# Optimization experiments

Measured on AMD Instinct MI355X. Metric: run time of the kernel, lower is better.

## Reference

```python
import jax, jax.numpy as jnp
import numpy as np

N_NODES = 50000
N_EDGES = 800000
D_IN = 128
D_OUT = 128


def setup_inputs() -> dict:
    key = jax.random.key(0)
    k_x, k_e, k_w, k_b = jax.random.split(key, 4)
    x = jax.random.normal(k_x, (N_NODES, D_IN), dtype=jnp.float32)
    edge_index = jax.random.randint(k_e, (2, N_EDGES), 0, N_NODES, dtype=jnp.int64)
    # nn.Linear(in_dim, out_dim): W is [out, in], b is [out]
    W = jax.random.normal(k_w, (D_OUT, D_IN), dtype=jnp.float32) * (1.0 / np.sqrt(D_IN))
    b = jax.random.normal(k_b, (D_OUT,), dtype=jnp.float32) * 0.01
    return {"x": x, "edge_index": edge_index, "W": W, "b": b}


def reference(x, edge_index, W, b):
    row, col = edge_index[0], edge_index[1]
    n = x.shape[0]
    # scatter-add of gathered source features: agg[row] += x[col]
    agg = jax.ops.segment_sum(x[col], row, num_segments=n)  # [N, d_in]
    # in-degree per destination node (bincount of row), clamped to >= 1
    deg = jax.ops.segment_sum(jnp.ones((row.shape[0],), dtype=x.dtype), row,
                              num_segments=n)
    deg = jnp.maximum(deg, 1.0)[:, None]  # [N, 1]
    agg = agg / deg
    # linear (y = agg @ W.T + b) then relu
    return jax.nn.relu(jnp.einsum('nd,od->no', agg, W) + b)
```

## Files before the change

kernel.cpp:

```cpp
#include <hip/hip_runtime.h>

#define N_NODES 50000
#define N_EDGES 800000
#define D 128

#define NCRS 196
#define CCAP 4608
#define EPB 2048
#define NEBLK ((N_EDGES + EPB - 1) / EPB)
#define NFB 3125
#define LCAP16 768
#define XN (N_NODES * D / 4)
#define WN (D * D / 4)
#define CVTBLK ((XN + WN + 255) / 256)

#define XB_OFF   0u
#define WB_OFF   12800000u
#define GCUR_OFF 12832768u
#define CRS_OFF  12833792u
#define WS_NEED_A (CRS_OFF + (unsigned)NCRS * CCAP * 4u)

#define CNT_OFF 0u
#define OFF_OFF 200704u
#define CUR_OFF 401920u
#define CSR_OFF 602112u
#define WT_OFF  3802112u
#define PART_OFF 3867648u
#define BASE_OFF 3868672u
#define WS_NEED_B (BASE_OFF + 1024u)

#define SCAN_B 256
#define SCAN_NBLK ((N_NODES + SCAN_B - 1) / SCAN_B)

using bf16x8 = __attribute__((ext_vector_type(8))) short;
using f32x4 = __attribute__((ext_vector_type(4))) float;

static __device__ __forceinline__ unsigned short bf16_rne(float f) {
  unsigned u = __float_as_uint(f);
  return (unsigned short)((u + 0x7fffu + ((u >> 16) & 1u)) >> 16);
}
static __device__ __forceinline__ unsigned pack_bf16(float a, float b) {
  return (unsigned)bf16_rne(a) | ((unsigned)bf16_rne(b) << 16);
}
static __device__ __forceinline__ float bf_lo(unsigned v) {
  return __uint_as_float(v << 16);
}
static __device__ __forceinline__ float bf_hi(unsigned v) {
  return __uint_as_float(v & 0xffff0000u);
}

static __device__ __forceinline__ unsigned wave_excl_scan_256(
    unsigned c, int t, unsigned* wsum) {
  unsigned xinc = c;
  #pragma unroll
  for (int o = 1; o < 64; o <<= 1) {
    unsigned n = __shfl_up(xinc, o, 64);
    if ((t & 63) >= o) xinc += n;
  }
  if ((t & 63) == 63) wsum[t >> 6] = xinc;
  __syncthreads();
  unsigned add = 0;
  #pragma unroll
  for (int w = 0; w < 4; ++w)
    if (w < (t >> 6)) add += wsum[w];
  return xinc - c + add;
}

__global__ __launch_bounds__(256) void zero_gcur(unsigned* __restrict__ gcur) {
  if (threadIdx.x < NCRS) gcur[threadIdx.x] = 0u;
}

__global__ __launch_bounds__(256) void phase1(
    const float4* __restrict__ x4, uint2* __restrict__ xb,
    const float4* __restrict__ w4, uint2* __restrict__ wb,
    const int* __restrict__ ei, unsigned* __restrict__ gcur,
    unsigned* __restrict__ crs) {
  const int t = threadIdx.x;

  if (blockIdx.x < NEBLK) {
    __shared__ unsigned ent[EPB];
    __shared__ unsigned srt[EPB];
    __shared__ unsigned s[256];
    __shared__ unsigned wsum[4];
    __shared__ unsigned offx[NCRS], cur[NCRS], gb[NCRS];
    const int base = blockIdx.x * EPB;
    const int n = (N_EDGES - base < EPB) ? (N_EDGES - base) : EPB;
    for (int i = t; i < n; i += 256) {
      unsigned dst = (unsigned)ei[base + i];
      unsigned src = (unsigned)ei[N_EDGES + base + i];
      ent[i] = ((dst >> 8) << 24) | (src << 8) | (dst & 255u);
    }
    s[t] = 0;
    __syncthreads();
    for (int i = t; i < n; i += 256) atomicAdd(&s[ent[i] >> 24], 1u);
    __syncthreads();
    unsigned c = s[t];
    unsigned ex = wave_excl_scan_256(c, t, wsum);
    if (t < NCRS) {
      offx[t] = ex;
      cur[t] = ex;
      if (c) gb[t] = atomicAdd(&gcur[t], c);
    }
    __syncthreads();
    for (int i = t; i < n; i += 256) {
      unsigned e = ent[i];
      unsigned pos = atomicAdd(&cur[e >> 24], 1u);
      srt[pos] = e;
    }
    __syncthreads();
    for (int i = t; i < n; i += 256) {
      unsigned e = srt[i];
      unsigned k = e >> 24;
      unsigned idx = gb[k] + ((unsigned)i - offx[k]);
      if (idx < CCAP) crs[k * CCAP + idx] = e;
    }
  } else {
    int i = (blockIdx.x - NEBLK) * 256 + t;
    if (i < XN) {
      float4 v = x4[i];
      uint2 r;
      r.x = pack_bf16(v.x, v.y);
      r.y = pack_bf16(v.z, v.w);
      xb[i] = r;
    } else if (i < XN + WN) {
      int j = i - XN;
      float4 v = w4[j];
      uint2 r;
      r.x = pack_bf16(v.x, v.y);
      r.y = pack_bf16(v.z, v.w);
      wb[j] = r;
    }
  }
}

__global__ __launch_bounds__(256) void sortbins(
    const unsigned* __restrict__ gcur, unsigned* __restrict__ crs) {
  __shared__ unsigned ent[CCAP];
  __shared__ unsigned cur[256];
  __shared__ unsigned wsum[4];
  const int t = threadIdx.x;
  const int c = blockIdx.x;
  unsigned n = gcur[c];
  n = (n > CCAP) ? CCAP : n;
  unsigned* region = crs + (unsigned)c * CCAP;

  for (unsigned i = t; i < n; i += 256) ent[i] = region[i];
  cur[t] = 0;
  __syncthreads();
  for (unsigned i = t; i < n; i += 256) atomicAdd(&cur[ent[i] & 255u], 1u);
  __syncthreads();
  unsigned cc = cur[t];
  unsigned ex = wave_excl_scan_256(cc, t, wsum);
  unsigned* offs = region + 2304;
  offs[t] = ex;
  if (t == 255) offs[256] = n;
  __syncthreads();
  cur[t] = ex;
  __syncthreads();
  unsigned short* lst = (unsigned short*)region;
  for (unsigned i = t; i < n; i += 256) {
    unsigned e = ent[i];
    unsigned pos = atomicAdd(&cur[e & 255u], 1u);
    lst[pos] = (unsigned short)((e >> 8) & 0xFFFFu);
  }
}

__global__ __launch_bounds__(256) void agg_gemm(
    const unsigned* __restrict__ xb, const unsigned short* __restrict__ wb,
    const unsigned* __restrict__ crs, const float* __restrict__ b,
    float* __restrict__ out) {
  __shared__ unsigned abuf[16 * 64];
  __shared__ unsigned short llst[LCAP16];
  __shared__ unsigned loffs[17];
  const int t = threadIdx.x;
  const int fb = blockIdx.x;
  const int coarse = fb >> 4;
  const int ln0 = (fb & 15) * 16;

  const unsigned* region = crs + (unsigned)coarse * CCAP;
  const unsigned* offs = region + 2304;
  const unsigned short* lst = (const unsigned short*)region;

  if (t < 17) loffs[t] = offs[ln0 + t];
  __syncthreads();
  const unsigned base = loffs[0];
  unsigned total = loffs[16] - base;
  if (total > LCAP16) total = LCAP16;
  for (unsigned i = t; i < total; i += 256) llst[i] = lst[base + i];
  __syncthreads();

  const int r = t >> 4;
  const int p4 = t & 15;
  const uint4* x4g = (const uint4*)xb;
  {
    unsigned beg = loffs[r] - base, end = loffs[r + 1] - base;
    float a0 = 0.f, a1 = 0.f, a2 = 0.f, a3 = 0.f;
    float a4 = 0.f, a5 = 0.f, a6 = 0.f, a7 = 0.f;
    unsigned j = beg;
    for (; j + 8 <= end; j += 8) {
      uint4 v0 = x4g[(size_t)llst[j] * 16 + p4];
      uint4 v1 = x4g[(size_t)llst[j + 1] * 16 + p4];
      uint4 v2 = x4g[(size_t)llst[j + 2] * 16 + p4];
      uint4 v3 = x4g[(size_t)llst[j + 3] * 16 + p4];
      uint4 v4 = x4g[(size_t)llst[j + 4] * 16 + p4];
      uint4 v5 = x4g[(size_t)llst[j + 5] * 16 + p4];
      uint4 v6 = x4g[(size_t)llst[j + 6] * 16 + p4];
      uint4 v7 = x4g[(size_t)llst[j + 7] * 16 + p4];
      a0 += (bf_lo(v0.x) + bf_lo(v1.x)) + (bf_lo(v2.x) + bf_lo(v3.x)) +
            ((bf_lo(v4.x) + bf_lo(v5.x)) + (bf_lo(v6.x) + bf_lo(v7.x)));
      a1 += (bf_hi(v0.x) + bf_hi(v1.x)) + (bf_hi(v2.x) + bf_hi(v3.x)) +
            ((bf_hi(v4.x) + bf_hi(v5.x)) + (bf_hi(v6.x) + bf_hi(v7.x)));
      a2 += (bf_lo(v0.y) + bf_lo(v1.y)) + (bf_lo(v2.y) + bf_lo(v3.y)) +
            ((bf_lo(v4.y) + bf_lo(v5.y)) + (bf_lo(v6.y) + bf_lo(v7.y)));
      a3 += (bf_hi(v0.y) + bf_hi(v1.y)) + (bf_hi(v2.y) + bf_hi(v3.y)) +
            ((bf_hi(v4.y) + bf_hi(v5.y)) + (bf_hi(v6.y) + bf_hi(v7.y)));
      a4 += (bf_lo(v0.z) + bf_lo(v1.z)) + (bf_lo(v2.z) + bf_lo(v3.z)) +
            ((bf_lo(v4.z) + bf_lo(v5.z)) + (bf_lo(v6.z) + bf_lo(v7.z)));
      a5 += (bf_hi(v0.z) + bf_hi(v1.z)) + (bf_hi(v2.z) + bf_hi(v3.z)) +
            ((bf_hi(v4.z) + bf_hi(v5.z)) + (bf_hi(v6.z) + bf_hi(v7.z)));
      a6 += (bf_lo(v0.w) + bf_lo(v1.w)) + (bf_lo(v2.w) + bf_lo(v3.w)) +
            ((bf_lo(v4.w) + bf_lo(v5.w)) + (bf_lo(v6.w) + bf_lo(v7.w)));
      a7 += (bf_hi(v0.w) + bf_hi(v1.w)) + (bf_hi(v2.w) + bf_hi(v3.w)) +
            ((bf_hi(v4.w) + bf_hi(v5.w)) + (bf_hi(v6.w) + bf_hi(v7.w)));
    }
    for (; j + 2 <= end; j += 2) {
      uint4 v0 = x4g[(size_t)llst[j] * 16 + p4];
      uint4 v1 = x4g[(size_t)llst[j + 1] * 16 + p4];
      a0 += bf_lo(v0.x) + bf_lo(v1.x);
      a1 += bf_hi(v0.x) + bf_hi(v1.x);
      a2 += bf_lo(v0.y) + bf_lo(v1.y);
      a3 += bf_hi(v0.y) + bf_hi(v1.y);
      a4 += bf_lo(v0.z) + bf_lo(v1.z);
      a5 += bf_hi(v0.z) + bf_hi(v1.z);
      a6 += bf_lo(v0.w) + bf_lo(v1.w);
      a7 += bf_hi(v0.w) + bf_hi(v1.w);
    }
    if (j < end) {
      uint4 v = x4g[(size_t)llst[j] * 16 + p4];
      a0 += bf_lo(v.x);
      a1 += bf_hi(v.x);
      a2 += bf_lo(v.y);
      a3 += bf_hi(v.y);
      a4 += bf_lo(v.z);
      a5 += bf_hi(v.z);
      a6 += bf_lo(v.w);
      a7 += bf_hi(v.w);
    }
    float inv = 1.0f / fmaxf((float)(end - beg), 1.0f);
    unsigned w0 = (unsigned)(4 * p4) ^ ((unsigned)(r & 7) << 2);
    *(uint4*)&abuf[r * 64 + w0] =
        make_uint4(pack_bf16(a0 * inv, a1 * inv), pack_bf16(a2 * inv, a3 * inv),
                   pack_bf16(a4 * inv, a5 * inv), pack_bf16(a6 * inv, a7 * inv));
  }
  __syncthreads();

  const int wave = t >> 6, lane = t & 63;
  const int arow = lane & 15, khi = lane >> 4;
  bf16x8 afrag[4];
  #pragma unroll
  for (int kb = 0; kb < 4; ++kb) {
    int w0 = (kb * 16 + khi * 4) ^ ((arow & 7) << 2);
    afrag[kb] = *(const bf16x8*)&abuf[arow * 64 + w0];
  }
  #pragma unroll
  for (int ct = 0; ct < 2; ++ct) {
    int o = wave * 32 + ct * 16 + arow;
    f32x4 acc = (f32x4){0.f, 0.f, 0.f, 0.f};
    #pragma unroll
    for (int kb = 0; kb < 4; ++kb) {
      bf16x8 bfrag = *(const bf16x8*)(wb + o * 128 + kb * 32 + khi * 8);
      acc = __builtin_amdgcn_mfma_f32_16x16x32_bf16(afrag[kb], bfrag, acc,
                                                    0, 0, 0);
    }
    float bias = b[o];
    #pragma unroll
    for (int rg = 0; rg < 4; ++rg) {
      int row = fb * 16 + khi * 4 + rg;
      out[(size_t)row * 128 + o] = fmaxf(acc[rg] + bias, 0.0f);
    }
  }
}

__global__ __launch_bounds__(256) void transpose_w(
    const float* __restrict__ W, float* __restrict__ Wt) {
  int i = blockIdx.x * 256 + threadIdx.x;
  if (i < D * D) {
    int o = i >> 7, d = i & 127;
    Wt[d * D + o] = W[i];
  }
}

__global__ __launch_bounds__(256) void count_kernel(
    const int* __restrict__ ei, unsigned* __restrict__ cnt) {
  int e = blockIdx.x * 256 + threadIdx.x;
  if (e < N_EDGES) atomicAdd(&cnt[ei[e]], 1u);
}

__global__ __launch_bounds__(256) void scan_p1(
    const unsigned* __restrict__ cnt, unsigned* __restrict__ partial) {
  int t = threadIdx.x;
  int g = blockIdx.x * SCAN_B + t;
  unsigned c = (g < N_NODES) ? cnt[g] : 0u;
  #pragma unroll
  for (int o = 32; o > 0; o >>= 1) c += __shfl_down(c, o, 64);
  __shared__ unsigned ws[4];
  if ((t & 63) == 0) ws[t >> 6] = c;
  __syncthreads();
  if (t == 0) partial[blockIdx.x] = ws[0] + ws[1] + ws[2] + ws[3];
}

__global__ __launch_bounds__(256) void scan_p2(
    const unsigned* __restrict__ partial, unsigned* __restrict__ base,
    unsigned* __restrict__ off) {
  __shared__ unsigned s[256];
  int t = threadIdx.x;
  unsigned v = (t < SCAN_NBLK) ? partial[t] : 0u;
  s[t] = v;
  __syncthreads();
  #pragma unroll
  for (int o = 1; o < 256; o <<= 1) {
    unsigned a = (t >= o) ? s[t - o] : 0u;
    __syncthreads();
    s[t] += a;
    __syncthreads();
  }
  if (t < SCAN_NBLK) base[t] = s[t] - v;
  if (t == 255) off[N_NODES] = s[255];
}

__global__ __launch_bounds__(256) void scan_p3(
    const unsigned* __restrict__ cnt, const unsigned* __restrict__ base,
    unsigned* __restrict__ off, unsigned* __restrict__ cur) {
  __shared__ unsigned s[256];
  int t = threadIdx.x;
  int g = blockIdx.x * SCAN_B + t;
  unsigned c = (g < N_NODES) ? cnt[g] : 0u;
  s[t] = c;
  __syncthreads();
  #pragma unroll
  for (int o = 1; o < 256; o <<= 1) {
    unsigned a = (t >= o) ? s[t - o] : 0u;
    __syncthreads();
    s[t] += a;
    __syncthreads();
  }
  if (g < N_NODES) {
    unsigned e = base[blockIdx.x] + s[t] - c;
    off[g] = e;
    cur[g] = e;
  }
}

__global__ __launch_bounds__(256) void fill_kernel(
    const int* __restrict__ ei, unsigned* __restrict__ cur,
    int* __restrict__ csr) {
  int e = blockIdx.x * 256 + threadIdx.x;
  if (e < N_EDGES) {
    int dst = ei[e];
    int src = ei[N_EDGES + e];
    unsigned pos = atomicAdd(&cur[dst], 1u);
    csr[pos] = src;
  }
}

__global__ __launch_bounds__(256) void aggregate_kernel(
    const float* __restrict__ x, const unsigned* __restrict__ off,
    const int* __restrict__ csr, float* __restrict__ agg) {
  int wave = (blockIdx.x * 256 + threadIdx.x) >> 6;
  int lane = threadIdx.x & 63;
  if (wave >= N_NODES) return;
  unsigned beg = off[wave], end = off[wave + 1];
  const float2* x2 = (const float2*)x;
  float ax = 0.f, ay = 0.f;
  unsigned i = beg;
  for (; i + 2 <= end; i += 2) {
    int s0 = csr[i], s1 = csr[i + 1];
    float2 v0 = x2[(size_t)s0 * 64 + lane];
    float2 v1 = x2[(size_t)s1 * 64 + lane];
    ax += v0.x + v1.x;
    ay += v0.y + v1.y;
  }
  if (i < end) {
    float2 v = x2[(size_t)csr[i] * 64 + lane];
    ax += v.x;
    ay += v.y;
  }
  float inv = 1.0f / fmaxf((float)(end - beg), 1.0f);
  float2 r;
  r.x = ax * inv;
  r.y = ay * inv;
  ((float2*)agg)[(size_t)wave * 64 + lane] = r;
}

__global__ __launch_bounds__(256) void gemm_relu_kernel(
    float* __restrict__ io, const float* __restrict__ deg,
    const float* __restrict__ Wt, const float* __restrict__ b) {
  __shared__ float a_lds[32 * 128];
  int tid = threadIdx.x;
  int row0 = blockIdx.x * 32;
  const float4* g4 = (const float4*)io + (size_t)row0 * 32;
  #pragma unroll
  for (int k = 0; k < 4; ++k) {
    int f = k * 256 + tid;
    int r = f >> 5;
    int grow = row0 + r;
    float4 v = make_float4(0.f, 0.f, 0.f, 0.f);
    float inv = 1.0f;
    if (grow < N_NODES) {
      v = g4[f];
      if (deg) inv = 1.0f / fmaxf(deg[grow], 1.0f);
    }
    float* dstp = &a_lds[f * 4];
    dstp[0] = v.x * inv;
    dstp[1] = v.y * inv;
    dstp[2] = v.z * inv;
    dstp[3] = v.w * inv;
  }
  __syncthreads();
  int cq = tid & 31;
  int rb = (tid >> 5) * 4;
  float acc[4][4] = {};
  const float4* Wt4 = (const float4*)Wt;
  #pragma unroll 4
  for (int d = 0; d < 128; ++d) {
    float4 w = Wt4[d * 32 + cq];
    #pragma unroll
    for (int i = 0; i < 4; ++i) {
      float a = a_lds[(rb + i) * 128 + d];
      acc[i][0] += a * w.x;
      acc[i][1] += a * w.y;
      acc[i][2] += a * w.z;
      acc[i][3] += a * w.w;
    }
  }
  float4 bb = ((const float4*)b)[cq];
  float4* out4 = (float4*)io;
  #pragma unroll
  for (int i = 0; i < 4; ++i) {
    int grow = row0 + rb + i;
    if (grow < N_NODES) {
      float4 r;
      r.x = fmaxf(acc[i][0] + bb.x, 0.0f);
      r.y = fmaxf(acc[i][1] + bb.y, 0.0f);
      r.z = fmaxf(acc[i][2] + bb.z, 0.0f);
      r.w = fmaxf(acc[i][3] + bb.w, 0.0f);
      out4[(size_t)grow * 32 + cq] = r;
    }
  }
}

__global__ __launch_bounds__(256) void scatter_kernel(
    const float* __restrict__ x, const int* __restrict__ ei,
    float* __restrict__ agg, float* __restrict__ deg) {
  int gid = blockIdx.x * 256 + threadIdx.x;
  int e = gid >> 5;
  if (e >= N_EDGES) return;
  int part = gid & 31;
  int dst = ei[e];
  int src = ei[N_EDGES + e];
  const float4* x4 = (const float4*)x;
  float4 v = x4[(size_t)src * 32 + part];
  float* base = agg + (size_t)dst * D + part * 4;
  atomicAdd(base + 0, v.x);
  atomicAdd(base + 1, v.y);
  atomicAdd(base + 2, v.z);
  atomicAdd(base + 3, v.w);
  if (part == 0) atomicAdd(deg + dst, 1.0f);
}

extern "C" void kernel_launch(void* const* d_in, const int* in_sizes, int n_in,
                              void* d_out, int out_size, void* d_ws, size_t ws_size,
                              hipStream_t stream) {
  const float* x = (const float*)d_in[0];
  const int* ei = (const int*)d_in[1];
  const float* W = (const float*)d_in[2];
  const float* b = (const float*)d_in[3];
  float* out = (float*)d_out;

  if (ws_size >= WS_NEED_A) {
    unsigned* xb = (unsigned*)((char*)d_ws + XB_OFF);
    unsigned short* wb = (unsigned short*)((char*)d_ws + WB_OFF);
    unsigned* gcur = (unsigned*)((char*)d_ws + GCUR_OFF);
    unsigned* crs = (unsigned*)((char*)d_ws + CRS_OFF);

    zero_gcur<<<1, 256, 0, stream>>>(gcur);
    phase1<<<NEBLK + CVTBLK, 256, 0, stream>>>(
        (const float4*)x, (uint2*)xb, (const float4*)W, (uint2*)wb,
        ei, gcur, crs);
    sortbins<<<NCRS, 256, 0, stream>>>(gcur, crs);
    agg_gemm<<<NFB, 256, 0, stream>>>(xb, wb, crs, b, out);
  } else if (ws_size >= WS_NEED_B) {
    unsigned* cnt = (unsigned*)((char*)d_ws + CNT_OFF);
    unsigned* off = (unsigned*)((char*)d_ws + OFF_OFF);
    unsigned* cur = (unsigned*)((char*)d_ws + CUR_OFF);
    int* csr = (int*)((char*)d_ws + CSR_OFF);
    float* Wt = (float*)((char*)d_ws + WT_OFF);
    unsigned* partial = (unsigned*)((char*)d_ws + PART_OFF);
    unsigned* base = (unsigned*)((char*)d_ws + BASE_OFF);

    hipMemsetAsync(cnt, 0, N_NODES * sizeof(unsigned), stream);
    transpose_w<<<(D * D + 255) / 256, 256, 0, stream>>>(W, Wt);
    count_kernel<<<(N_EDGES + 255) / 256, 256, 0, stream>>>(ei, cnt);
    scan_p1<<<SCAN_NBLK, 256, 0, stream>>>(cnt, partial);
    scan_p2<<<1, 256, 0, stream>>>(partial, base, off);
    scan_p3<<<SCAN_NBLK, 256, 0, stream>>>(cnt, base, off, cur);
    fill_kernel<<<(N_EDGES + 255) / 256, 256, 0, stream>>>(ei, cur, csr);
    aggregate_kernel<<<(N_NODES * 64 + 255) / 256, 256, 0, stream>>>(
        x, off, csr, out);
    gemm_relu_kernel<<<(N_NODES + 31) / 32, 256, 0, stream>>>(
        out, nullptr, Wt, b);
  } else {
    float* deg = (float*)d_ws;
    float* Wt = (float*)((char*)d_ws + 256 * 1024);
    hipMemsetAsync(d_out, 0, (size_t)N_NODES * D * sizeof(float), stream);
    hipMemsetAsync(deg, 0, N_NODES * sizeof(float), stream);
    transpose_w<<<(D * D + 255) / 256, 256, 0, stream>>>(W, Wt);
    scatter_kernel<<<(N_EDGES * 32) / 256, 256, 0, stream>>>(x, ei, out, deg);
    gemm_relu_kernel<<<(N_NODES + 31) / 32, 256, 0, stream>>>(out, deg, Wt, b);
  }
}
```

Baseline: 70.46 us.

## Split bf16 conversion across binning and sort kernels to balance load

The fp32-to-bf16 conversion of x and W, previously done entirely in the binning kernel, is now split. The first 2048 blocks' worth of items stay in the binning kernel and the rest move into extra blocks of the per-bin sort kernel. The sort kernel has only 196 blocks and would otherwise leave most of the GPU idle, so the moved work can fill those idle compute units. The cost is a heavier sort launch, and the sort blocks may now queue behind conversion blocks.

```diff
diff --git a/kernel.cpp b/kernel.cpp
--- a/kernel.cpp
+++ b/kernel.cpp
@@ -12,7 +12,11 @@
 #define LCAP16 768
 #define XN (N_NODES * D / 4)
 #define WN (D * D / 4)
-#define CVTBLK ((XN + WN + 255) / 256)
+#define CVT_TOT (XN + WN)
+#define CVTA_BLK 2048
+#define CVTA_ITEMS (CVTA_BLK * 256)
+#define CVTB_ITEMS (CVT_TOT - CVTA_ITEMS)
+#define CVTB_BLK ((CVTB_ITEMS + 255) / 256)
 
 #define XB_OFF   0u
 #define WB_OFF   12800000u
@@ -49,6 +53,25 @@
   return __uint_as_float(v & 0xffff0000u);
 }
 
+static __device__ __forceinline__ void convert_item(
+    int i, const float4* __restrict__ x4, uint2* __restrict__ xb,
+    const float4* __restrict__ w4, uint2* __restrict__ wb) {
+  if (i < XN) {
+    float4 v = x4[i];
+    uint2 r;
+    r.x = pack_bf16(v.x, v.y);
+    r.y = pack_bf16(v.z, v.w);
+    xb[i] = r;
+  } else if (i < CVT_TOT) {
+    int j = i - XN;
+    float4 v = w4[j];
+    uint2 r;
+    r.x = pack_bf16(v.x, v.y);
+    r.y = pack_bf16(v.z, v.w);
+    wb[j] = r;
+  }
+}
+
 static __device__ __forceinline__ unsigned wave_excl_scan_256(
     unsigned c, int t, unsigned* wsum) {
   unsigned xinc = c;
@@ -70,7 +93,7 @@
   if (threadIdx.x < NCRS) gcur[threadIdx.x] = 0u;
 }
 
-__global__ __launch_bounds__(256) void phase1(
+__global__ __launch_bounds__(256) void bin_convA(
     const float4* __restrict__ x4, uint2* __restrict__ xb,
     const float4* __restrict__ w4, uint2* __restrict__ wb,
     const int* __restrict__ ei, unsigned* __restrict__ gcur,
@@ -115,53 +138,46 @@
       if (idx < CCAP) crs[k * CCAP + idx] = e;
     }
   } else {
-    int i = (blockIdx.x - NEBLK) * 256 + t;
-    if (i < XN) {
-      float4 v = x4[i];
-      uint2 r;
-      r.x = pack_bf16(v.x, v.y);
-      r.y = pack_bf16(v.z, v.w);
-      xb[i] = r;
-    } else if (i < XN + WN) {
-      int j = i - XN;
-      float4 v = w4[j];
-      uint2 r;
-      r.x = pack_bf16(v.x, v.y);
-      r.y = pack_bf16(v.z, v.w);
-      wb[j] = r;
-    }
-  }
-}
-
-__global__ __launch_bounds__(256) void sortbins(
+    convert_item((blockIdx.x - NEBLK) * 256 + t, x4, xb, w4, wb);
+  }
+}
+
+__global__ __launch_bounds__(256) void sort_convB(
+    const float4* __restrict__ x4, uint2* __restrict__ xb,
+    const float4* __restrict__ w4, uint2* __restrict__ wb,
     const unsigned* __restrict__ gcur, unsigned* __restrict__ crs) {
-  __shared__ unsigned ent[CCAP];
-  __shared__ unsigned cur[256];
-  __shared__ unsigned wsum[4];
   const int t = threadIdx.x;
-  const int c = blockIdx.x;
-  unsigned n = gcur[c];
-  n = (n > CCAP) ? CCAP : n;
-  unsigned* region = crs + (unsigned)c * CCAP;
-
-  for (unsigned i = t; i < n; i += 256) ent[i] = region[i];
-  cur[t] = 0;
-  __syncthreads();
-  for (unsigned i = t; i < n; i += 256) atomicAdd(&cur[ent[i] & 255u], 1u);
-  __syncthreads();
-  unsigned cc = cur[t];
-  unsigned ex = wave_excl_scan_256(cc, t, wsum);
-  unsigned* offs = region + 2304;
-  offs[t] = ex;
-  if (t == 255) offs[256] = n;
-  __syncthreads();
-  cur[t] = ex;
-  __syncthreads();
-  unsigned short* lst = (unsigned short*)region;
-  for (unsigned i = t; i < n; i += 256) {
-    unsigned e = ent[i];
-    unsigned pos = atomicAdd(&cur[e & 255u], 1u);
-    lst[pos] = (unsigned short)((e >> 8) & 0xFFFFu);
+
+  if (blockIdx.x < NCRS) {
+    __shared__ unsigned ent[CCAP];
+    __shared__ unsigned cur[256];
+    __shared__ unsigned wsum[4];
+    const int c = blockIdx.x;
+    unsigned n = gcur[c];
+    n = (n > CCAP) ? CCAP : n;
+    unsigned* region = crs + (unsigned)c * CCAP;
+
+    for (unsigned i = t; i < n; i += 256) ent[i] = region[i];
+    cur[t] = 0;
+    __syncthreads();
+    for (unsigned i = t; i < n; i += 256) atomicAdd(&cur[ent[i] & 255u], 1u);
+    __syncthreads();
+    unsigned cc = cur[t];
+    unsigned ex = wave_excl_scan_256(cc, t, wsum);
+    unsigned* offs = region + 2304;
+    offs[t] = ex;
+    if (t == 255) offs[256] = n;
+    __syncthreads();
+    cur[t] = ex;
+    __syncthreads();
+    unsigned short* lst = (unsigned short*)region;
+    for (unsigned i = t; i < n; i += 256) {
+      unsigned e = ent[i];
+      unsigned pos = atomicAdd(&cur[e & 255u], 1u);
+      lst[pos] = (unsigned short)((e >> 8) & 0xFFFFu);
+    }
+  } else {
+    convert_item(CVTA_ITEMS + (blockIdx.x - NCRS) * 256 + t, x4, xb, w4, wb);
   }
 }
 
@@ -484,10 +500,12 @@
     unsigned* crs = (unsigned*)((char*)d_ws + CRS_OFF);
 
     zero_gcur<<<1, 256, 0, stream>>>(gcur);
-    phase1<<<NEBLK + CVTBLK, 256, 0, stream>>>(
+    bin_convA<<<NEBLK + CVTA_BLK, 256, 0, stream>>>(
         (const float4*)x, (uint2*)xb, (const float4*)W, (uint2*)wb,
         ei, gcur, crs);
-    sortbins<<<NCRS, 256, 0, stream>>>(gcur, crs);
+    sort_convB<<<NCRS + CVTB_BLK, 256, 0, stream>>>(
+        (const float4*)x, (uint2*)xb, (const float4*)W, (uint2*)wb,
+        gcur, crs);
     agg_gemm<<<NFB, 256, 0, stream>>>(xb, wb, crs, b, out);
   } else if (ws_size >= WS_NEED_B) {
     unsigned* cnt = (unsigned*)((char*)d_ws + CNT_OFF);
```

After: 70.36 us. No clear change (-0.1%).
